# Performance work log

Measured on AMD Instinct MI355X. Metric: run time of the kernel, lower is better.

The kernel has to match this reference:

```python
import jax, jax.numpy as jnp
import numpy as np

B, T, D, F, E = 8, 2048, 1024, 4096, 16
C_FACTOR = 1.25
LB_W = 0.01


def setup_inputs() -> dict:
    key = jax.random.key(0)
    ks = jax.random.split(key, 4)
    x = jax.random.normal(ks[0], (B, T, D), dtype=jnp.float32)
    Wr = jax.random.normal(ks[1], (E, D), dtype=jnp.float32) * 0.02
    W1 = jax.random.normal(ks[2], (E, F, D), dtype=jnp.float32) * 0.02
    b1 = jnp.zeros((E, F), dtype=jnp.float32)
    W2 = jax.random.normal(ks[3], (E, D, F), dtype=jnp.float32) * 0.02
    b2 = jnp.zeros((E, D), dtype=jnp.float32)
    return {"x": x, "Wr": Wr, "W1": W1, "b1": b1, "W2": W2, "b2": b2}


def reference(x, Wr, W1, b1, W2, b2):
    Bs, Ts, Ds = x.shape
    Es = Wr.shape[0]
    tokens = Bs * Ts
    xf = x.reshape(tokens, Ds)

    # router
    logits = xf @ Wr.T                       # [tokens, E]
    probs = jax.nn.softmax(logits, axis=-1)
    top1 = jnp.argmax(probs, axis=-1)        # [tokens]
    top1p = jnp.max(probs, axis=-1)          # [tokens]

    capacity = int(C_FACTOR * tokens / Es)   # static python int

    onehot = jax.nn.one_hot(top1, Es, dtype=jnp.int32)        # [tokens, E]
    f = onehot.sum(axis=0).astype(probs.dtype) / tokens
    p = probs.mean(axis=0)
    lb_loss = Es * jnp.sum(f * p) * LB_W

    # faithful reproduction of idx[::expert_capacity]: among tokens routed to
    # expert e (in token order), keep only those whose rank % capacity == 0
    ranks = jnp.cumsum(onehot, axis=0) - 1                     # [tokens, E]
    keep = (onehot == 1) & (ranks % capacity == 0)             # [tokens, E]
    K = (tokens - 1) // capacity + 1                           # static max kept per expert

    idx = jax.vmap(lambda m: jnp.nonzero(m, size=K, fill_value=0)[0])(keep.T)  # [E, K]
    valid = jnp.take_along_axis(keep.T, idx, axis=1)           # [E, K] bool

    xg = xf[idx]                                               # [E, K, D]
    h = jax.nn.gelu(jnp.einsum('ekd,efd->ekf', xg, W1) + b1[:, None, :], approximate=False)
    eo = jnp.einsum('ekf,edf->ekd', h, W2) + b2[:, None, :]    # [E, K, D]
    scale = top1p[idx] * valid.astype(eo.dtype)                # [E, K]
    eo = eo * scale[..., None]

    out = jnp.zeros_like(xf).at[idx.reshape(-1)].add(eo.reshape(-1, Ds))
    return out.reshape(Bs, Ts, Ds), lb_loss
```

## Files before the change

### kernel.cpp

```cpp
#include <hip/hip_runtime.h>
#include <math.h>


#define TOKENS 16384
#define DD     1024
#define FF     4096
#define EE     16
#define CAP    1280
#define KMAX   13
#define NBLK   256

__global__ __launch_bounds__(256) void router_kernel(
    const float* __restrict__ x, const float* __restrict__ Wr,
    int* __restrict__ top1, float* __restrict__ top1p,
    int* __restrict__ blockhist, float* __restrict__ blockpsum)
{
    __shared__ float wrj[EE * 256];
    __shared__ float p_acc[EE];
    __shared__ int   hist[EE];

    const int tid  = threadIdx.x;
    const int wave = tid >> 6;
    const int lane = tid & 63;
    const int blk  = blockIdx.x;

    if (tid < EE) { p_acc[tid] = 0.0f; hist[tid] = 0; }

    for (int it = 0; it < 4; ++it) {
        const int tbase = blk * 64 + wave * 16 + it * 4;

        float4 xr[4][4];
        #pragma unroll
        for (int t = 0; t < 4; ++t) {
            const float4* xp = (const float4*)(x + (size_t)(tbase + t) * DD);
            #pragma unroll
            for (int j = 0; j < 4; ++j) xr[t][j] = xp[j * 64 + lane];
        }

        float acc[4][EE];
        #pragma unroll
        for (int t = 0; t < 4; ++t)
            #pragma unroll
            for (int e = 0; e < EE; ++e) acc[t][e] = 0.0f;

        for (int j = 0; j < 4; ++j) {
            __syncthreads();
            #pragma unroll
            for (int k = 0; k < 4; ++k) {
                int i = tid + k * 256;
                int e = i >> 6, c = i & 63;
                ((float4*)wrj)[i] = ((const float4*)Wr)[e * 256 + j * 64 + c];
            }
            __syncthreads();
            #pragma unroll
            for (int e = 0; e < EE; ++e) {
                float4 w = ((const float4*)(wrj + e * 256))[lane];
                #pragma unroll
                for (int t = 0; t < 4; ++t) {
                    acc[t][e] += xr[t][j].x * w.x + xr[t][j].y * w.y
                               + xr[t][j].z * w.z + xr[t][j].w * w.w;
                }
            }
        }

        #pragma unroll
        for (int t = 0; t < 4; ++t)
            #pragma unroll
            for (int e = 0; e < EE; ++e) {
                float v = acc[t][e];
                v += __shfl_xor(v, 32);
                v += __shfl_xor(v, 16);
                v += __shfl_xor(v, 8);
                v += __shfl_xor(v, 4);
                v += __shfl_xor(v, 2);
                v += __shfl_xor(v, 1);
                acc[t][e] = v;
            }

        if (lane < 4) {
            float lg[EE];
            #pragma unroll
            for (int e = 0; e < EE; ++e) {
                float v = acc[3][e];
                if (lane == 2) v = acc[2][e];
                if (lane == 1) v = acc[1][e];
                if (lane == 0) v = acc[0][e];
                lg[e] = v;
            }
            const int gt = tbase + lane;
            float mx = lg[0]; int bi = 0;
            #pragma unroll
            for (int e = 1; e < EE; ++e)
                if (lg[e] > mx) { mx = lg[e]; bi = e; }
            float pr[EE];
            float s = 0.0f;
            #pragma unroll
            for (int e = 0; e < EE; ++e) { pr[e] = expf(lg[e] - mx); s += pr[e]; }
            const float inv = 1.0f / s;
            top1[gt]  = bi;
            top1p[gt] = inv;
            #pragma unroll
            for (int e = 0; e < EE; ++e) atomicAdd(&p_acc[e], pr[e] * inv);
            atomicAdd(&hist[bi], 1);
        }
    }
    __syncthreads();
    if (tid < EE) {
        blockhist[blk * EE + tid] = hist[tid];
        blockpsum[blk * EE + tid] = p_acc[tid];
    }
}

__global__ __launch_bounds__(256) void scan_kernel(
    const int* __restrict__ blockhist, const float* __restrict__ blockpsum,
    int* __restrict__ base, int* __restrict__ nkept,
    const int* __restrict__ top1, float* __restrict__ mult0,
    float* __restrict__ lb_out)
{
    __shared__ int   hist_l[NBLK * EE];
    __shared__ int   gsum[EE * 16];
    __shared__ float fps[EE * 16];
    __shared__ float fp[EE];
    __shared__ int   nk_l[EE];

    const int tid = threadIdx.x;
    for (int i = tid; i < NBLK * EE; i += 256) hist_l[i] = blockhist[i];
    __syncthreads();

    const int e = tid >> 4, g = tid & 15;
    int s = 0;
    float sp = 0.0f;
    for (int b = g * 16; b < g * 16 + 16; ++b) {
        s  += hist_l[b * EE + e];
        sp += blockpsum[b * EE + e];
    }
    gsum[e * 16 + g] = s;
    fps[e * 16 + g]  = sp;
    __syncthreads();

    int pre = 0;
    for (int g2 = 0; g2 < g; ++g2) pre += gsum[e * 16 + g2];
    int run = pre;
    for (int b = g * 16; b < g * 16 + 16; ++b) {
        base[b * EE + e] = run;
        run += hist_l[b * EE + e];
    }
    if (g == 15) {
        const int c = run;
        const int nk = (c > 0) ? ((c - 1) / CAP + 1) : 0;
        nkept[e] = nk;
        nk_l[e]  = nk;
        float ps = 0.0f;
        for (int g2 = 0; g2 < 16; ++g2) ps += fps[e * 16 + g2];
        fp[e] = ((float)c / (float)TOKENS) * (ps / (float)TOKENS);
    }
    __syncthreads();
    if (tid == 0) {
        const int e0 = top1[0];
        mult0[0] = (float)(1 + KMAX - nk_l[e0]);
        float sum = 0.0f;
        for (int i = 0; i < EE; ++i) sum += fp[i];
        lb_out[0] = (float)EE * sum * 0.01f;
    }
}

__global__ __launch_bounds__(64) void keep_kernel(
    const int* __restrict__ top1, const float* __restrict__ top1p,
    const int* __restrict__ base, const float* __restrict__ mult0,
    int* __restrict__ kept_tok, float* __restrict__ kept_scale,
    int* __restrict__ slotmap)
{
    __shared__ int t1[64];
    const int tid = threadIdx.x;
    const int blk = blockIdx.x;
    const int gt  = blk * 64 + tid;
    const int e   = top1[gt];
    t1[tid] = e;
    __syncthreads();
    int r = 0;
    for (int i = 0; i < tid; ++i) r += (t1[i] == e) ? 1 : 0;
    const int rank = base[blk * EE + e] + r;
    int sm = -1;
    if (rank % CAP == 0) {
        const int slot = rank / CAP;
        sm = e * KMAX + slot;
        kept_tok[sm] = gt;
        float sc = top1p[gt];
        if (gt == 0) sc *= mult0[0];
        kept_scale[sm] = sc;
    }
    slotmap[gt] = sm;
}

__global__ __launch_bounds__(256) void expert1_kernel(
    const float* __restrict__ x, const float* __restrict__ W1,
    const float* __restrict__ b1, const int* __restrict__ nkept,
    const int* __restrict__ kept_tok, float* __restrict__ h)
{
    const int e    = blockIdx.x >> 8;
    const int fblk = blockIdx.x & 255;
    const int ne   = nkept[e];
    if (ne == 0) return;
    const int wave = threadIdx.x >> 6;
    const int lane = threadIdx.x & 63;

    for (int s = 0; s < ne; ++s) {
        const int t = kept_tok[e * KMAX + s];
        const float4* xp = (const float4*)(x + (size_t)t * DD);
        #pragma unroll
        for (int i = 0; i < 4; ++i) {
            const int f = fblk * 16 + wave * 4 + i;
            const float4* wrow = (const float4*)(W1 + ((size_t)e * FF + f) * DD);
            float d = 0.0f;
            #pragma unroll
            for (int k = 0; k < 4; ++k) {
                const float4 w  = wrow[k * 64 + lane];
                const float4 xv = xp[k * 64 + lane];
                d += w.x*xv.x + w.y*xv.y + w.z*xv.z + w.w*xv.w;
            }
            d += __shfl_xor(d, 32);
            d += __shfl_xor(d, 16);
            d += __shfl_xor(d, 8);
            d += __shfl_xor(d, 4);
            d += __shfl_xor(d, 2);
            d += __shfl_xor(d, 1);
            if (lane == 0) {
                const float v = d + b1[e * FF + f];
                h[((size_t)e * KMAX + s) * FF + f] =
                    0.5f * v * (1.0f + erff(v * 0.70710678118654752440f));
            }
        }
    }
}

__global__ __launch_bounds__(256) void expert2_kernel(
    const float* __restrict__ h, const float* __restrict__ W2,
    const float* __restrict__ b2, const int* __restrict__ nkept,
    const float* __restrict__ kept_scale, float* __restrict__ eo)
{
    const int e    = blockIdx.x >> 8;
    const int dblk = blockIdx.x & 255;
    const int ne   = nkept[e];
    if (ne == 0) return;
    const int wave = threadIdx.x >> 6;
    const int lane = threadIdx.x & 63;
    const int d    = dblk * 4 + wave;

    const float4* wrow = (const float4*)(W2 + ((size_t)e * DD + d) * FF);
    for (int s = 0; s < ne; ++s) {
        const float4* hp = (const float4*)(h + ((size_t)e * KMAX + s) * FF);
        float acc = 0.0f;
        #pragma unroll
        for (int k = 0; k < 16; ++k) {
            const float4 w  = wrow[k * 64 + lane];
            const float4 hv = hp[k * 64 + lane];
            acc += w.x*hv.x + w.y*hv.y + w.z*hv.z + w.w*hv.w;
        }
        acc += __shfl_xor(acc, 32);
        acc += __shfl_xor(acc, 16);
        acc += __shfl_xor(acc, 8);
        acc += __shfl_xor(acc, 4);
        acc += __shfl_xor(acc, 2);
        acc += __shfl_xor(acc, 1);
        if (lane == 0) {
            const float sc = kept_scale[e * KMAX + s];
            eo[((size_t)e * KMAX + s) * DD + d] = sc * (acc + b2[e * DD + d]);
        }
    }
}

__global__ __launch_bounds__(256) void expand_kernel(
    const float* __restrict__ eo, const int* __restrict__ slotmap,
    float* __restrict__ out)
{
    const int nf4 = TOKENS * DD / 4;
    int idx = blockIdx.x * 256 + threadIdx.x;
    const int stride = 4096 * 256;
    for (; idx < nf4; idx += stride) {
        const int t    = idx >> 8;
        const int slot = slotmap[t];
        float4 v = make_float4(0.0f, 0.0f, 0.0f, 0.0f);
        if (slot >= 0) v = ((const float4*)eo)[slot * 256 + (idx & 255)];
        ((float4*)out)[idx] = v;
    }
}

extern "C" void kernel_launch(void* const* d_in, const int* in_sizes, int n_in,
                              void* d_out, int out_size, void* d_ws, size_t ws_size,
                              hipStream_t stream) {
    const float* x  = (const float*)d_in[0];
    const float* Wr = (const float*)d_in[1];
    const float* W1 = (const float*)d_in[2];
    const float* b1 = (const float*)d_in[3];
    const float* W2 = (const float*)d_in[4];
    const float* b2 = (const float*)d_in[5];
    float* out = (float*)d_out;

    char* p = (char*)d_ws;
    int*   top1       = (int*)p;    p += (size_t)TOKENS * 4;
    float* top1p      = (float*)p;  p += (size_t)TOKENS * 4;
    int*   slotmap    = (int*)p;    p += (size_t)TOKENS * 4;
    int*   blockhist  = (int*)p;    p += (size_t)NBLK * EE * 4;
    float* blockpsum  = (float*)p;  p += (size_t)NBLK * EE * 4;
    int*   base       = (int*)p;    p += (size_t)NBLK * EE * 4;
    int*   nkept      = (int*)p;    p += 256;
    float* mult0      = (float*)p;  p += 256;
    int*   kept_tok   = (int*)p;    p += 1024;
    float* kept_scale = (float*)p;  p += 1024;
    float* eo         = (float*)p;  p += (size_t)EE * KMAX * DD * 4;
    float* h          = (float*)p;  p += (size_t)EE * KMAX * FF * 4;
    (void)ws_size; (void)in_sizes; (void)n_in;

    router_kernel<<<NBLK, 256, 0, stream>>>(x, Wr, top1, top1p,
                                            blockhist, blockpsum);
    scan_kernel<<<1, 256, 0, stream>>>(blockhist, blockpsum, base, nkept,
                                       top1, mult0, out + (size_t)out_size - 1);
    keep_kernel<<<NBLK, 64, 0, stream>>>(top1, top1p, base, mult0,
                                         kept_tok, kept_scale, slotmap);
    expert1_kernel<<<EE * 256, 256, 0, stream>>>(x, W1, b1, nkept, kept_tok, h);
    expert2_kernel<<<EE * 256, 256, 0, stream>>>(h, W2, b2, nkept, kept_scale, eo);
    expand_kernel<<<4096, 256, 0, stream>>>(eo, slotmap, out);
}
```

Baseline: 667.9 us.

## Restructure router to stage Wr in halves and double block count

```diff
diff --git a/kernel.cpp b/kernel.cpp
--- a/kernel.cpp
+++ b/kernel.cpp
@@ -8,14 +8,14 @@
 #define EE     16
 #define CAP    1280
 #define KMAX   13
-#define NBLK   256
+#define NBLK   512
 
 __global__ __launch_bounds__(256) void router_kernel(
     const float* __restrict__ x, const float* __restrict__ Wr,
     int* __restrict__ top1, float* __restrict__ top1p,
     int* __restrict__ blockhist, float* __restrict__ blockpsum)
 {
-    __shared__ float wrj[EE * 256];
+    __shared__ float wr_l[8 * DD];
     __shared__ float p_acc[EE];
     __shared__ int   hist[EE];
 
@@ -26,65 +26,76 @@
 
     if (tid < EE) { p_acc[tid] = 0.0f; hist[tid] = 0; }
 
-    for (int it = 0; it < 4; ++it) {
-        const int tbase = blk * 64 + wave * 16 + it * 4;
-
-        float4 xr[4][4];
+    float acc[2][4][EE];
+    float4 xr[2][4][4];
+
+    #pragma unroll
+    for (int it = 0; it < 2; ++it) {
+        const int tbase = blk * 32 + wave * 8 + it * 4;
         #pragma unroll
         for (int t = 0; t < 4; ++t) {
             const float4* xp = (const float4*)(x + (size_t)(tbase + t) * DD);
             #pragma unroll
-            for (int j = 0; j < 4; ++j) xr[t][j] = xp[j * 64 + lane];
-        }
-
-        float acc[4][EE];
+            for (int j = 0; j < 4; ++j) xr[it][t][j] = xp[j * 64 + lane];
+        }
         #pragma unroll
         for (int t = 0; t < 4; ++t)
             #pragma unroll
-            for (int e = 0; e < EE; ++e) acc[t][e] = 0.0f;
-
+            for (int e = 0; e < EE; ++e) acc[it][t][e] = 0.0f;
+    }
+
+    #pragma unroll
+    for (int half = 0; half < 2; ++half) {
+        if (half) __syncthreads();
+        #pragma unroll
+        for (int i = 0; i < 8; ++i)
+            ((float4*)wr_l)[i * 256 + tid] =
+                ((const float4*)Wr)[half * 2048 + i * 256 + tid];
+        __syncthreads();
+
+        #pragma unroll
         for (int j = 0; j < 4; ++j) {
-            __syncthreads();
-            #pragma unroll
-            for (int k = 0; k < 4; ++k) {
-                int i = tid + k * 256;
-                int e = i >> 6, c = i & 63;
-                ((float4*)wrj)[i] = ((const float4*)Wr)[e * 256 + j * 64 + c];
-            }
-            __syncthreads();
+            #pragma unroll
+            for (int eh = 0; eh < 8; ++eh) {
+                const int e = half * 8 + eh;
+                const float4 w = ((const float4*)(wr_l + eh * DD))[j * 64 + lane];
+                #pragma unroll
+                for (int it = 0; it < 2; ++it) {
+                    acc[it][0][e] += xr[it][0][j].x*w.x + xr[it][0][j].y*w.y + xr[it][0][j].z*w.z + xr[it][0][j].w*w.w;
+                    acc[it][1][e] += xr[it][1][j].x*w.x + xr[it][1][j].y*w.y + xr[it][1][j].z*w.z + xr[it][1][j].w*w.w;
+                    acc[it][2][e] += xr[it][2][j].x*w.x + xr[it][2][j].y*w.y + xr[it][2][j].z*w.z + xr[it][2][j].w*w.w;
+                    acc[it][3][e] += xr[it][3][j].x*w.x + xr[it][3][j].y*w.y + xr[it][3][j].z*w.z + xr[it][3][j].w*w.w;
+                }
+            }
+        }
+    }
+
+    #pragma unroll
+    for (int it = 0; it < 2; ++it) {
+        const int tbase = blk * 32 + wave * 8 + it * 4;
+
+        #pragma unroll
+        for (int t = 0; t < 4; ++t)
             #pragma unroll
             for (int e = 0; e < EE; ++e) {
-                float4 w = ((const float4*)(wrj + e * 256))[lane];
-                #pragma unroll
-                for (int t = 0; t < 4; ++t) {
-                    acc[t][e] += xr[t][j].x * w.x + xr[t][j].y * w.y
-                               + xr[t][j].z * w.z + xr[t][j].w * w.w;
-                }
-            }
-        }
-
-        #pragma unroll
-        for (int t = 0; t < 4; ++t)
-            #pragma unroll
-            for (int e = 0; e < EE; ++e) {
-                float v = acc[t][e];
+                float v = acc[it][t][e];
                 v += __shfl_xor(v, 32);
                 v += __shfl_xor(v, 16);
                 v += __shfl_xor(v, 8);
                 v += __shfl_xor(v, 4);
                 v += __shfl_xor(v, 2);
                 v += __shfl_xor(v, 1);
-                acc[t][e] = v;
+                acc[it][t][e] = v;
             }
 
         if (lane < 4) {
             float lg[EE];
             #pragma unroll
             for (int e = 0; e < EE; ++e) {
-                float v = acc[3][e];
-                if (lane == 2) v = acc[2][e];
-                if (lane == 1) v = acc[1][e];
-                if (lane == 0) v = acc[0][e];
+                float v = acc[it][3][e];
+                if (lane == 2) v = acc[it][2][e];
+                if (lane == 1) v = acc[it][1][e];
+                if (lane == 0) v = acc[it][0][e];
                 lg[e] = v;
             }
             const int gt = tbase + lane;
@@ -130,7 +141,7 @@
     const int e = tid >> 4, g = tid & 15;
     int s = 0;
     float sp = 0.0f;
-    for (int b = g * 16; b < g * 16 + 16; ++b) {
+    for (int b = g * 32; b < g * 32 + 32; ++b) {
         s  += hist_l[b * EE + e];
         sp += blockpsum[b * EE + e];
     }
@@ -141,7 +152,7 @@
     int pre = 0;
     for (int g2 = 0; g2 < g; ++g2) pre += gsum[e * 16 + g2];
     int run = pre;
-    for (int b = g * 16; b < g * 16 + 16; ++b) {
+    for (int b = g * 32; b < g * 32 + 32; ++b) {
         base[b * EE + e] = run;
         run += hist_l[b * EE + e];
     }
@@ -177,9 +188,11 @@
     const int e   = top1[gt];
     t1[tid] = e;
     __syncthreads();
+    const int start = tid & 32;
     int r = 0;
-    for (int i = 0; i < tid; ++i) r += (t1[i] == e) ? 1 : 0;
-    const int rank = base[blk * EE + e] + r;
+    for (int i = start; i < tid; ++i) r += (t1[i] == e) ? 1 : 0;
+    const int hb   = gt >> 5;
+    const int rank = base[hb * EE + e] + r;
     int sm = -1;
     if (rank % CAP == 0) {
         const int slot = rank / CAP;
@@ -315,8 +328,8 @@
                                             blockhist, blockpsum);
     scan_kernel<<<1, 256, 0, stream>>>(blockhist, blockpsum, base, nkept,
                                        top1, mult0, out + (size_t)out_size - 1);
-    keep_kernel<<<NBLK, 64, 0, stream>>>(top1, top1p, base, mult0,
-                                         kept_tok, kept_scale, slotmap);
+    keep_kernel<<<256, 64, 0, stream>>>(top1, top1p, base, mult0,
+                                        kept_tok, kept_scale, slotmap);
     expert1_kernel<<<EE * 256, 256, 0, stream>>>(x, W1, b1, nkept, kept_tok, h);
     expert2_kernel<<<EE * 256, 256, 0, stream>>>(h, W2, b2, nkept, kept_scale, eo);
     expand_kernel<<<4096, 256, 0, stream>>>(eo, slotmap, out);
```

Result: slower. 694.3 us (+4.0%).
